# Performance work log

Hardware: AMD Instinct MI355X
Metric: run time of the kernel (lower is better)

The kernel has to match this reference:

```python
import jax, jax.numpy as jnp
import numpy as np

# Module config (from init_kwargs)
HIDDEN = 1024
NUM_HEADS = 16
HEAD_DIM = HIDDEN // NUM_HEADS  # 64
SCALE = HEAD_DIM ** -0.5
INF = jnp.finfo(jnp.float32).max  # tf uses dtype.max as the masking constant

T, B, S = 8, 16, 4096  # tgt_len, bsz, cached src_len


def setup_inputs() -> dict:
    key = jax.random.key(0)
    ks = jax.random.split(key, 9)
    glorot = (6.0 / (HIDDEN + HIDDEN)) ** 0.5
    return {
        "query_input": jax.random.normal(ks[0], (T, B, HIDDEN), jnp.float32),
        "prev_key": jax.random.normal(ks[1], (B, NUM_HEADS, S, HEAD_DIM), jnp.float32),
        "prev_value": jax.random.normal(ks[2], (B, NUM_HEADS, S, HEAD_DIM), jnp.float32),
        "key_padding_mask": jax.random.randint(ks[3], (B, S), 0, 2, jnp.int32),
        "new_state_order": jax.random.randint(ks[4], (B,), 0, B, jnp.int32),
        "Wq": jax.random.uniform(ks[5], (HIDDEN, HIDDEN), jnp.float32, -glorot, glorot),
        "bq": jnp.zeros((HIDDEN,), jnp.float32),
        "Wo": jax.random.uniform(ks[6], (HIDDEN, HIDDEN), jnp.float32, -glorot, glorot),
        "bo": jnp.zeros((HIDDEN,), jnp.float32),
    }


def reference(query_input, prev_key, prev_value, key_padding_mask, new_state_order, Wq, bq, Wo, bo):
    t, b, d = query_input.shape
    # q projection: tf.matmul(x, W, transpose_b=True) with W (in, hidden) -> x @ W.T
    q = (query_input @ Wq.T + bq) * SCALE          # (t, b, d)
    q = q.reshape(t, b, NUM_HEADS, HEAD_DIM).transpose(1, 2, 0, 3)  # (b, h, t, hd)
    # KV cache beam reorder (gather along batch)
    k = prev_key[new_state_order]                  # (b, h, s, hd)
    v = prev_value[new_state_order]                # (b, h, s, hd)
    scores = jnp.einsum('bhtd,bhsd->bhts', q, k)   # (b, h, t, s)
    # additive large-constant masking exactly as the tf code (scores - INF * mask)
    scores = scores - INF * key_padding_mask[:, None, None, :].astype(scores.dtype)
    attn = jax.nn.softmax(scores, axis=-1)
    out = jnp.einsum('bhts,bhsd->bhtd', attn, v)   # (b, h, t, hd)
    out = out.transpose(2, 0, 1, 3).reshape(t, b, d)  # (t, b, hidden)
    return out @ Wo.T + bo
```

## Files before the change

### kernel.cpp

```cpp
#include <hip/hip_runtime.h>
#include <hip/hip_bf16.h>
#include <math.h>

#define TLEN 8
#define BATCH 16
#define NH 16
#define HD 64
#define SLEN 4096
#define HID 1024
#define SPLITS 4
#define QSCALE 0.125f

#define DPP_ADD(p, ctrl)                                                     \
    do {                                                                     \
        int _t = __builtin_amdgcn_update_dpp(0, __float_as_int(p), (ctrl),   \
                                             0xF, 0xF, true);                \
        (p) += __int_as_float(_t);                                           \
    } while (0)

__global__ __launch_bounds__(256) void proj_kernel(
    const float* __restrict__ X, const float* __restrict__ W,
    const float* __restrict__ bias, float scale, float* __restrict__ out)
{
    __shared__ float xs[128][68];
    __shared__ float wt[4][68];
    const int tid = threadIdx.x;
    const int col = tid & 3;
    const int rg  = tid >> 2;
    const int c0 = blockIdx.x * 4;
    float acc0 = 0.f, acc1 = 0.f;

    for (int k0 = 0; k0 < HID; k0 += 64) {
        __syncthreads();
#pragma unroll
        for (int j = 0; j < 8; ++j) {
            int idx = tid + 256 * j;
            int r = idx >> 4, c4 = (idx & 15) * 4;
            *(float4*)&xs[r][c4] = *(const float4*)&X[(size_t)r * HID + k0 + c4];
        }
        if (tid < 64) {
            int r = tid >> 4, c4 = (tid & 15) * 4;
            *(float4*)&wt[r][c4] = *(const float4*)&W[(size_t)(c0 + r) * HID + k0 + c4];
        }
        __syncthreads();
#pragma unroll
        for (int kk = 0; kk < 64; kk += 4) {
            float4 w4 = *(const float4*)&wt[col][kk];
            float4 x0 = *(const float4*)&xs[2 * rg][kk];
            float4 x1 = *(const float4*)&xs[2 * rg + 1][kk];
            acc0 = fmaf(x0.x, w4.x, acc0); acc0 = fmaf(x0.y, w4.y, acc0);
            acc0 = fmaf(x0.z, w4.z, acc0); acc0 = fmaf(x0.w, w4.w, acc0);
            acc1 = fmaf(x1.x, w4.x, acc1); acc1 = fmaf(x1.y, w4.y, acc1);
            acc1 = fmaf(x1.z, w4.z, acc1); acc1 = fmaf(x1.w, w4.w, acc1);
        }
    }
    float bb = bias[c0 + col];
    out[(size_t)(2 * rg) * HID + c0 + col]     = (acc0 + bb) * scale;
    out[(size_t)(2 * rg + 1) * HID + c0 + col] = (acc1 + bb) * scale;
}

__global__ __launch_bounds__(256) void attn_partial_kernel(
    const float* __restrict__ Kg, const float* __restrict__ Vg,
    const int* __restrict__ mask, const int* __restrict__ order,
    const float* __restrict__ qbuf, float* __restrict__ pacc,
    float* __restrict__ pl)
{
    const int split = blockIdx.x;
    const int bh = blockIdx.y;
    const int b = bh >> 4, h = bh & 15;
    const int tid = threadIdx.x;
    const int wave = tid >> 6, lane = tid & 63;
    const int d0 = (lane & 15) * 4;

    float4 ql[TLEN];
#pragma unroll
    for (int t = 0; t < TLEN; ++t)
        ql[t] = *(const float4*)&qbuf[(size_t)(t * BATCH + b) * HID + h * HD + d0];

    const int bsrc = order[b];
    const size_t base4 = (size_t)(bsrc * NH + h) * SLEN * (HD / 4);
    const int kbase = split * (SLEN / SPLITS) + wave * (SLEN / SPLITS / 4);
    const float4* kp = (const float4*)Kg + base4 + (size_t)kbase * (HD / 4) + lane;
    const float4* vp = (const float4*)Vg + base4 + (size_t)kbase * (HD / 4) + lane;
    const int* mp = mask + (size_t)b * SLEN + kbase + (lane >> 4);

    float lsum[TLEN];
    float acc[TLEN][4];
#pragma unroll
    for (int t = 0; t < TLEN; ++t) {
        lsum[t] = 0.f;
        acc[t][0] = acc[t][1] = acc[t][2] = acc[t][3] = 0.f;
    }

    const float4 fz = make_float4(0.f, 0.f, 0.f, 0.f);

    int ma = mp[0], mb = mp[4];
    int m1a = mp[8], m1b = mp[12];
    float4 ka = fz, kb = fz, va = fz, vb = fz;
    if (!ma) { ka = kp[0];  va = vp[0]; }
    if (!mb) { kb = kp[64]; vb = vp[64]; }

#define BODY(KA, KB, VA, VB, MA, MB)                                         \
    do {                                                                     \
        _Pragma("unroll")                                                    \
        for (int t = 0; t < TLEN; ++t) {                                     \
            float pa_ = ql[t].x * (KA).x + ql[t].y * (KA).y +                \
                        ql[t].z * (KA).z + ql[t].w * (KA).w;                 \
            float pb_ = ql[t].x * (KB).x + ql[t].y * (KB).y +                \
                        ql[t].z * (KB).z + ql[t].w * (KB).w;                 \
            DPP_ADD(pa_, 0xB1);  DPP_ADD(pb_, 0xB1);                         \
            DPP_ADD(pa_, 0x4E);  DPP_ADD(pb_, 0x4E);                         \
            DPP_ADD(pa_, 0x141); DPP_ADD(pb_, 0x141);                        \
            DPP_ADD(pa_, 0x140); DPP_ADD(pb_, 0x140);                        \
            float ea = (MA) ? 0.f : __expf(pa_);                             \
            float eb = (MB) ? 0.f : __expf(pb_);                             \
            lsum[t] += ea + eb;                                              \
            acc[t][0] = fmaf(ea, (VA).x, acc[t][0]);                         \
            acc[t][1] = fmaf(ea, (VA).y, acc[t][1]);                         \
            acc[t][2] = fmaf(ea, (VA).z, acc[t][2]);                         \
            acc[t][3] = fmaf(ea, (VA).w, acc[t][3]);                         \
            acc[t][0] = fmaf(eb, (VB).x, acc[t][0]);                         \
            acc[t][1] = fmaf(eb, (VB).y, acc[t][1]);                         \
            acc[t][2] = fmaf(eb, (VB).z, acc[t][2]);                         \
            acc[t][3] = fmaf(eb, (VB).w, acc[t][3]);                         \
        }                                                                    \
    } while (0)

    for (int it = 0; it < 31; ++it) {
        int m2a = 1, m2b = 1;
        if (it < 30) { m2a = mp[(it + 2) * 8]; m2b = mp[(it + 2) * 8 + 4]; }
        const int nb4 = (it + 1) * 128;
        float4 nka = fz, nkb = fz, nva = fz, nvb = fz;
        if (!m1a) { nka = kp[nb4];      nva = vp[nb4]; }
        if (!m1b) { nkb = kp[nb4 + 64]; nvb = vp[nb4 + 64]; }

        BODY(ka, kb, va, vb, ma, mb);

        ka = nka; kb = nkb; va = nva; vb = nvb;
        ma = m1a; mb = m1b; m1a = m2a; m1b = m2b;
    }
    BODY(ka, kb, va, vb, ma, mb);

#pragma unroll
    for (int t = 0; t < TLEN; ++t) {
#pragma unroll
        for (int j = 0; j < 4; ++j) {
            acc[t][j] += __shfl_xor(acc[t][j], 16);
            acc[t][j] += __shfl_xor(acc[t][j], 32);
        }
        lsum[t] += __shfl_xor(lsum[t], 16);
        lsum[t] += __shfl_xor(lsum[t], 32);
    }

    const int p = split * 4 + wave;
    if (lane < 16) {
        float* pa = pacc + (size_t)(bh * 16 + p) * TLEN * HD;
#pragma unroll
        for (int t = 0; t < TLEN; ++t) {
            float4 v;
            v.x = acc[t][0]; v.y = acc[t][1]; v.z = acc[t][2]; v.w = acc[t][3];
            *(float4*)&pa[t * HD + d0] = v;
        }
        if (lane == 0) {
#pragma unroll
            for (int t = 0; t < TLEN; ++t)
                pl[(size_t)(bh * 16 + p) * TLEN + t] = lsum[t];
        }
    }
#undef BODY
}

__global__ __launch_bounds__(512) void combine_kernel(
    const float* __restrict__ pacc, const float* __restrict__ pl,
    float* __restrict__ otmp)
{
    const int bh = blockIdx.x, b = bh >> 4, h = bh & 15;
    const int i = threadIdx.x;
    const int t = i >> 6, d = i & 63;
    float a = 0.f, l = 0.f;
#pragma unroll
    for (int p = 0; p < 16; ++p) {
        a += pacc[((size_t)(bh * 16 + p) * TLEN + t) * HD + d];
        l += pl[(size_t)(bh * 16 + p) * TLEN + t];
    }
    otmp[(size_t)(t * BATCH + b) * HID + h * HD + d] = a / l;
}

extern "C" void kernel_launch(void* const* d_in, const int* in_sizes, int n_in,
                              void* d_out, int out_size, void* d_ws, size_t ws_size,
                              hipStream_t stream) {
    const float* x     = (const float*)d_in[0];
    const float* pk    = (const float*)d_in[1];
    const float* pv    = (const float*)d_in[2];
    const int*   mask  = (const int*)d_in[3];
    const int*   order = (const int*)d_in[4];
    const float* Wq    = (const float*)d_in[5];
    const float* bq    = (const float*)d_in[6];
    const float* Wo    = (const float*)d_in[7];
    const float* bo    = (const float*)d_in[8];
    float* out = (float*)d_out;

    float* ws   = (float*)d_ws;
    float* qbuf = ws;
    float* pacc = qbuf + 128 * 1024;
    float* plw  = pacc + 256 * 16 * TLEN * HD;
    float* otmp = plw + 256 * 16 * TLEN;

    proj_kernel<<<256, 256, 0, stream>>>(x, Wq, bq, QSCALE, qbuf);
    attn_partial_kernel<<<dim3(SPLITS, 256), 256, 0, stream>>>(
        pk, pv, mask, order, qbuf, pacc, plw);
    combine_kernel<<<256, 512, 0, stream>>>(pacc, plw, otmp);
    proj_kernel<<<256, 256, 0, stream>>>(otmp, Wo, bo, 1.0f, out);
}
```

Baseline: 136.6 us.

## Compact unmasked key indices and balance attention work over valid positions

Adds a prefix-scan kernel that builds, per batch, a compacted list of unmasked key positions and their count. The attention kernel then walks only those indices, splitting them evenly across the 16 waves per (b,h), so masked positions cost no loop iterations and the load is balanced. In exchange it adds an extra kernel launch, an indirect index load per key row, and gathered K/V reads that are less contiguous than before. Fully masked rows would give zero sums, as they could before.

```diff
diff --git a/kernel.cpp b/kernel.cpp
--- a/kernel.cpp
+++ b/kernel.cpp
@@ -59,17 +59,49 @@
     out[(size_t)(2 * rg + 1) * HID + c0 + col] = (acc1 + bb) * scale;
 }
 
+__global__ __launch_bounds__(256) void compact_kernel(
+    const int* __restrict__ mask, int* __restrict__ cidx, int* __restrict__ ccnt)
+{
+    const int b = blockIdx.x;
+    const int tid = threadIdx.x;
+    __shared__ int ssum[256];
+    const int* mrow = mask + (size_t)b * SLEN;
+    int loc[16];
+    int cnt = 0;
+#pragma unroll
+    for (int j = 0; j < 16; ++j) {
+        loc[j] = mrow[tid * 16 + j];
+        cnt += (loc[j] == 0);
+    }
+    ssum[tid] = cnt;
+    __syncthreads();
+    for (int off = 1; off < 256; off <<= 1) {
+        int v = (tid >= off) ? ssum[tid - off] : 0;
+        __syncthreads();
+        ssum[tid] += v;
+        __syncthreads();
+    }
+    int pos = ssum[tid] - cnt;
+    int* outr = cidx + (size_t)b * SLEN;
+#pragma unroll
+    for (int j = 0; j < 16; ++j) {
+        if (loc[j] == 0) outr[pos++] = tid * 16 + j;
+    }
+    if (tid == 255) ccnt[b] = ssum[255];
+}
+
 __global__ __launch_bounds__(256) void attn_partial_kernel(
     const float* __restrict__ Kg, const float* __restrict__ Vg,
-    const int* __restrict__ mask, const int* __restrict__ order,
-    const float* __restrict__ qbuf, float* __restrict__ pacc,
-    float* __restrict__ pl)
+    const int* __restrict__ cidx, const int* __restrict__ ccnt,
+    const int* __restrict__ order, const float* __restrict__ qbuf,
+    float* __restrict__ pacc, float* __restrict__ pl)
 {
     const int split = blockIdx.x;
     const int bh = blockIdx.y;
     const int b = bh >> 4, h = bh & 15;
     const int tid = threadIdx.x;
     const int wave = tid >> 6, lane = tid & 63;
+    const int g = lane >> 4;
     const int d0 = (lane & 15) * 4;
 
     float4 ql[TLEN];
@@ -78,11 +110,16 @@
         ql[t] = *(const float4*)&qbuf[(size_t)(t * BATCH + b) * HID + h * HD + d0];
 
     const int bsrc = order[b];
+    const int cnt = ccnt[b];
     const size_t base4 = (size_t)(bsrc * NH + h) * SLEN * (HD / 4);
-    const int kbase = split * (SLEN / SPLITS) + wave * (SLEN / SPLITS / 4);
-    const float4* kp = (const float4*)Kg + base4 + (size_t)kbase * (HD / 4) + lane;
-    const float4* vp = (const float4*)Vg + base4 + (size_t)kbase * (HD / 4) + lane;
-    const int* mp = mask + (size_t)b * SLEN + kbase + (lane >> 4);
+    const float4* kg4 = (const float4*)Kg;
+    const float4* vg4 = (const float4*)Vg;
+
+    const int p = split * 4 + wave;
+    const int chunk = (((cnt + 15) >> 4) + 7) & ~7;
+    const int iters = chunk >> 3;
+    const int wstart = p * chunk;
+    const int* crow = cidx + (size_t)b * SLEN;
 
     float lsum[TLEN];
     float acc[TLEN][4];
@@ -92,16 +129,29 @@
         acc[t][0] = acc[t][1] = acc[t][2] = acc[t][3] = 0.f;
     }
 
-    const float4 fz = make_float4(0.f, 0.f, 0.f, 0.f);
-
-    int ma = mp[0], mb = mp[4];
-    int m1a = mp[8], m1b = mp[12];
-    float4 ka = fz, kb = fz, va = fz, vb = fz;
-    if (!ma) { ka = kp[0];  va = vp[0]; }
-    if (!mb) { kb = kp[64]; vb = vp[64]; }
-
-#define BODY(KA, KB, VA, VB, MA, MB)                                         \
+#define LOAD_IDX(J, IA, IB)                                                  \
+    {                                                                        \
+        int pa_ = wstart + (J) * 8 + g;                                      \
+        int pb_ = pa_ + 4;                                                   \
+        (IA) = crow[pa_ < 4095 ? pa_ : 4095];                                \
+        (IB) = crow[pb_ < 4095 ? pb_ : 4095];                                \
+    }
+
+#define LOAD_KV(J, IA, IB, KA, VA, KB, VB)                                   \
+    {                                                                        \
+        int pa_ = wstart + (J) * 8 + g;                                      \
+        int ia_ = (pa_ < cnt) ? (IA) : 0;                                    \
+        int ib_ = (pa_ + 4 < cnt) ? (IB) : 0;                                \
+        size_t aa_ = base4 + (size_t)ia_ * (HD / 4) + (lane & 15);           \
+        size_t ab_ = base4 + (size_t)ib_ * (HD / 4) + (lane & 15);           \
+        (KA) = kg4[aa_]; (VA) = vg4[aa_];                                    \
+        (KB) = kg4[ab_]; (VB) = vg4[ab_];                                    \
+    }
+
+#define BODY(IT, KA, KB, VA, VB)                                             \
     do {                                                                     \
+        const int inA = (wstart + (IT) * 8 + g) >= cnt;                      \
+        const int inB = (wstart + (IT) * 8 + 4 + g) >= cnt;                  \
         _Pragma("unroll")                                                    \
         for (int t = 0; t < TLEN; ++t) {                                     \
             float pa_ = ql[t].x * (KA).x + ql[t].y * (KA).y +                \
@@ -112,8 +162,8 @@
             DPP_ADD(pa_, 0x4E);  DPP_ADD(pb_, 0x4E);                         \
             DPP_ADD(pa_, 0x141); DPP_ADD(pb_, 0x141);                        \
             DPP_ADD(pa_, 0x140); DPP_ADD(pb_, 0x140);                        \
-            float ea = (MA) ? 0.f : __expf(pa_);                             \
-            float eb = (MB) ? 0.f : __expf(pb_);                             \
+            float ea = inA ? 0.f : __expf(pa_);                              \
+            float eb = inB ? 0.f : __expf(pb_);                              \
             lsum[t] += ea + eb;                                              \
             acc[t][0] = fmaf(ea, (VA).x, acc[t][0]);                         \
             acc[t][1] = fmaf(ea, (VA).y, acc[t][1]);                         \
@@ -126,20 +176,27 @@
         }                                                                    \
     } while (0)
 
-    for (int it = 0; it < 31; ++it) {
-        int m2a = 1, m2b = 1;
-        if (it < 30) { m2a = mp[(it + 2) * 8]; m2b = mp[(it + 2) * 8 + 4]; }
-        const int nb4 = (it + 1) * 128;
-        float4 nka = fz, nkb = fz, nva = fz, nvb = fz;
-        if (!m1a) { nka = kp[nb4];      nva = vp[nb4]; }
-        if (!m1b) { nkb = kp[nb4 + 64]; nvb = vp[nb4 + 64]; }
-
-        BODY(ka, kb, va, vb, ma, mb);
-
-        ka = nka; kb = nkb; va = nva; vb = nvb;
-        ma = m1a; mb = m1b; m1a = m2a; m1b = m2b;
-    }
-    BODY(ka, kb, va, vb, ma, mb);
+    if (iters > 0) {
+        int ia0, ib0, ia1, ib1;
+        LOAD_IDX(0, ia0, ib0);
+        LOAD_IDX(1, ia1, ib1);
+        float4 ka, kb, va, vb;
+        LOAD_KV(0, ia0, ib0, ka, va, kb, vb);
+
+        for (int it = 0; it < iters - 1; ++it) {
+            int nia, nib;
+            LOAD_IDX(it + 2, nia, nib);
+            float4 nka, nkb, nva, nvb;
+            LOAD_KV(it + 1, ia1, ib1, nka, nva, nkb, nvb);
+            BODY(it, ka, kb, va, vb);
+            ka = nka; kb = nkb; va = nva; vb = nvb;
+            ia1 = nia; ib1 = nib;
+        }
+        BODY(iters - 1, ka, kb, va, vb);
+    }
+#undef LOAD_IDX
+#undef LOAD_KV
+#undef BODY
 
 #pragma unroll
     for (int t = 0; t < TLEN; ++t) {
@@ -152,7 +209,6 @@
         lsum[t] += __shfl_xor(lsum[t], 32);
     }
 
-    const int p = split * 4 + wave;
     if (lane < 16) {
         float* pa = pacc + (size_t)(bh * 16 + p) * TLEN * HD;
 #pragma unroll
@@ -167,7 +223,6 @@
                 pl[(size_t)(bh * 16 + p) * TLEN + t] = lsum[t];
         }
     }
-#undef BODY
 }
 
 __global__ __launch_bounds__(512) void combine_kernel(
@@ -192,7 +247,7 @@
     const float* x     = (const float*)d_in[0];
     const float* pk    = (const float*)d_in[1];
     const float* pv    = (const float*)d_in[2];
-    const int*   mask  = (const int*)d_in[3];
+    const int*   maskp = (const int*)d_in[3];
     const int*   order = (const int*)d_in[4];
     const float* Wq    = (const float*)d_in[5];
     const float* bq    = (const float*)d_in[6];
@@ -205,10 +260,13 @@
     float* pacc = qbuf + 128 * 1024;
     float* plw  = pacc + 256 * 16 * TLEN * HD;
     float* otmp = plw + 256 * 16 * TLEN;
-
+    int*   cidx = (int*)(otmp + 128 * 1024);
+    int*   ccnt = cidx + 16 * SLEN;
+
+    compact_kernel<<<16, 256, 0, stream>>>(maskp, cidx, ccnt);
     proj_kernel<<<256, 256, 0, stream>>>(x, Wq, bq, QSCALE, qbuf);
     attn_partial_kernel<<<dim3(SPLITS, 256), 256, 0, stream>>>(
-        pk, pv, mask, order, qbuf, pacc, plw);
+        pk, pv, cidx, ccnt, order, qbuf, pacc, plw);
     combine_kernel<<<256, 512, 0, stream>>>(pacc, plw, otmp);
     proj_kernel<<<256, 256, 0, stream>>>(otmp, Wo, bo, 1.0f, out);
 }
```

After: 110.4 us (median of 2 runs). 19.2% less time.
